# Optimization experiments

Measured on AMD Instinct MI355X. Metric: run time of the kernel, lower is better.

The kernel has to match this reference:

```python
import jax, jax.numpy as jnp
import numpy as np

EPS = 0.01          # layer_norm_epsilon from Gpt2Config
ROPE_THETA = 10000.0


def _rms_norm(x, w, eps=EPS):
    # RmsNorm over the last (head_size) axis, computed in fp32
    var = jnp.mean(jnp.square(x.astype(jnp.float32)), axis=-1, keepdims=True)
    return (x.astype(jnp.float32) * jax.lax.rsqrt(var + eps)).astype(x.dtype) * w


def _rope_cos_sin(seq_len, head_size, dtype):
    # default (NeoX/llama-style) rotary embeddings over the full head dim
    inv_freq = 1.0 / (ROPE_THETA ** (jnp.arange(0, head_size, 2, dtype=jnp.float32) / head_size))
    ang = jnp.arange(seq_len, dtype=jnp.float32)[:, None] * inv_freq[None, :]   # [S, D/2]
    cos = jnp.concatenate([jnp.cos(ang), jnp.cos(ang)], axis=-1).astype(dtype)  # [S, D]
    sin = jnp.concatenate([jnp.sin(ang), jnp.sin(ang)], axis=-1).astype(dtype)
    return cos, sin


def _rotate_half(x):
    half = x.shape[-1] // 2
    return jnp.concatenate([-x[..., half:], x[..., :half]], axis=-1)


def _apply_rope(x, cos, sin):
    # x: [B, S, H, D]; cos/sin: [S, D]
    return x * cos[None, :, None, :] + _rotate_half(x) * sin[None, :, None, :]


def setup_inputs() -> dict:
    key = jax.random.key(0)
    ks = jax.random.split(key, 3)
    B, S, E, H, D = 4, 2048, 2048, 16, 128
    x = jax.random.normal(ks[0], (B, S, E), dtype=jnp.float32)
    w_qkv = jax.random.normal(ks[1], (E, 3, H, D), dtype=jnp.float32) * 0.02
    w_proj = jax.random.normal(ks[2], (H, D, E), dtype=jnp.float32) * 0.02
    q_norm_w = jnp.ones((D,), dtype=jnp.float32)
    k_norm_w = jnp.ones((D,), dtype=jnp.float32)
    return {"x": x, "w_qkv": w_qkv, "w_proj": w_proj,
            "q_norm_w": q_norm_w, "k_norm_w": k_norm_w}


def reference(x, w_qkv, w_proj, q_norm_w, k_norm_w):
    B, S, E = x.shape
    _, _, H, D = w_qkv.shape

    # fused QKV projection (no bias)
    qkv = jnp.einsum('bse,ekhd->kbshd', x, w_qkv)  # [3, B, S, H, D]
    q, k, v = qkv[0], qkv[1], qkv[2]

    # qk RmsNorm over head_size
    q = _rms_norm(q, q_norm_w)
    k = _rms_norm(k, k_norm_w)

    # rotary embeddings
    cos, sin = _rope_cos_sin(S, D, x.dtype)
    q = _apply_rope(q, cos, sin)
    k = _apply_rope(k, cos, sin)

    # scaled dot-product attention, upcast to fp32, causal mask
    scale = 1.0 / jnp.sqrt(jnp.float32(D))
    scores = jnp.einsum('bshd,bthd->bhst', q.astype(jnp.float32),
                        k.astype(jnp.float32)) * scale        # [B, H, S, S]
    causal = jnp.arange(S)[:, None] >= jnp.arange(S)[None, :]  # [S, S]
    scores = jnp.where(causal[None, None], scores, jnp.float32(-1e9))
    attn = jax.nn.softmax(scores, axis=-1).astype(x.dtype)

    out = jnp.einsum('bhst,bthd->bshd', attn, v)               # [B, S, H, D]
    y = jnp.einsum('bshd,hde->bse', out, w_proj)               # output projection
    return y
```

## Files before the change

### kernel.cpp

```cpp
#include <hip/hip_runtime.h>
#include <hip/hip_bf16.h>
#include <math.h>

typedef unsigned short u16;
typedef __attribute__((ext_vector_type(8))) short short8;
typedef __attribute__((ext_vector_type(4))) float f32x4;
typedef __attribute__((ext_vector_type(4))) unsigned short ushort4v;
typedef __attribute__((ext_vector_type(8))) unsigned short ushort8v;

#define DEV static __device__ __forceinline__

DEV u16 f2bf(float f) {
    unsigned int x = __builtin_bit_cast(unsigned int, f);
    x += 0x7fffu + ((x >> 16) & 1u);
    return (u16)(x >> 16);
}
DEV float bf2f(u16 u) {
    unsigned int x = ((unsigned int)u) << 16;
    return __builtin_bit_cast(float, x);
}
DEV unsigned int pk_bf_trunc(float lo, float hi) {
    return __builtin_amdgcn_perm(__builtin_bit_cast(unsigned int, hi),
                                 __builtin_bit_cast(unsigned int, lo), 0x07060302u);
}

DEV void gl_lds16(const u16* g, u16* l) {
    __builtin_amdgcn_global_load_lds(
        (const __attribute__((address_space(1))) void*)g,
        (__attribute__((address_space(3))) void*)l, 16, 0, 0);
}

DEV short8 ldsv(const u16* p) { return *(const short8*)p; }

__global__ __launch_bounds__(256) void k_x2bf(
    const float* __restrict__ in, u16* __restrict__ out)
{
    int idx = blockIdx.x * 256 + threadIdx.x;
    const float4* p = (const float4*)in + (size_t)idx * 2;
    float4 a = p[0], b = p[1];
    ushort8v v;
    v[0] = f2bf(a.x); v[1] = f2bf(a.y); v[2] = f2bf(a.z); v[3] = f2bf(a.w);
    v[4] = f2bf(b.x); v[5] = f2bf(b.y); v[6] = f2bf(b.z); v[7] = f2bf(b.w);
    *(ushort8v*)(out + (size_t)idx * 8) = v;
}

__global__ __launch_bounds__(256) void k_transpose_bf16(
    const float* __restrict__ in, u16* __restrict__ out, int R, int C)
{
    __shared__ u16 t[64][72];
    int r0 = blockIdx.y * 64, c0 = blockIdx.x * 64;
    int tid = threadIdx.x;
    for (int i = 0; i < 4; ++i) {
        int u = tid + i * 256;
        int r = u >> 4, c4 = (u & 15) * 4;
        const float4 v = *(const float4*)(in + (size_t)(r0 + r) * C + c0 + c4);
        t[c4 + 0][r] = f2bf(v.x); t[c4 + 1][r] = f2bf(v.y);
        t[c4 + 2][r] = f2bf(v.z); t[c4 + 3][r] = f2bf(v.w);
    }
    __syncthreads();
    for (int i = 0; i < 4; ++i) {
        int u = tid + i * 256;
        int c = u >> 4, r4 = (u & 15) * 4;
        ushort4v v;
        v[0] = t[c][r4]; v[1] = t[c][r4 + 1]; v[2] = t[c][r4 + 2]; v[3] = t[c][r4 + 3];
        *(ushort4v*)(out + (size_t)(c0 + c) * R + r0 + r4) = v;
    }
}

template <int MODE>
__global__ __launch_bounds__(512, 2) void k_gemm256(
    const u16* __restrict__ A, const u16* __restrict__ Bt,
    u16* __restrict__ outQ, u16* __restrict__ outK, u16* __restrict__ outV,
    float* __restrict__ outF, int M, int N, int K)
{
    __shared__ u16 sA[2][2][128 * 64];
    __shared__ u16 sB[2][2][128 * 64];
    const int tid = threadIdx.x;
    const int lane = tid & 63, wid = tid >> 6;
    const int wm = wid >> 2, wn = wid & 3;
    const int lm = lane & 15, lq = lane >> 4;
    const int row0 = blockIdx.y * 256, col0 = blockIdx.x * 256;

    const int rl = lane >> 3;
    const int clog = (lane & 7) ^ rl;
    const u16* gA = A  + (size_t)(row0 + rl) * K + clog * 8;
    const u16* gB = Bt + (size_t)(col0 + rl) * K + clog * 8;
    const int rg = wid * 16;

    auto stA = [&](int bb, int h, int kt) {
        const u16* g = gA + (size_t)(h * 128 + rg) * K + (size_t)kt * 64;
        u16* l = &sA[bb][h][rg * 64];
        gl_lds16(g, l);
        gl_lds16(g + (size_t)8 * K, l + 512);
    };
    auto stB = [&](int bb, int h, int kt) {
        const u16* g = gB + (size_t)(h * 128 + rg) * K + (size_t)kt * 64;
        u16* l = &sB[bb][h][rg * 64];
        gl_lds16(g, l);
        gl_lds16(g + (size_t)8 * K, l + 512);
    };

    const int sw  = lm & 7;
    const int axr = lm * 64;
    const int bxr = ((wn & 1) * 64 + lm) * 64;
    const int co0 = ((lq ^ sw) << 3);
    const int co1 = (((lq | 4) ^ sw) << 3);

    f32x4 acc[8][4];
#pragma unroll
    for (int a = 0; a < 8; ++a)
#pragma unroll
        for (int b = 0; b < 4; ++b) acc[a][b] = (f32x4){0.f, 0.f, 0.f, 0.f};

    short8 af[4][2], bf[4][2];
    const int NT = K >> 6;

    stB(0, 0, 0); stB(0, 1, 0); stA(0, 0, 0); stA(0, 1, 0);
    stB(1, 0, 1); stB(1, 1, 1);
    asm volatile("s_waitcnt vmcnt(4)" ::: "memory");
    __builtin_amdgcn_s_barrier();

    auto tile_step = [&](int T, int buf) {
        const u16* pA = &sA[buf][wm][0];
        const u16* pB = &sB[buf][wn >> 1][0];
        const int nb = buf ^ 1;
        const bool p1ok = (T + 1 < NT);
        const bool p2ok = (T + 2 < NT);

#pragma unroll
        for (int t = 0; t < 4; ++t) {
            af[t][0] = ldsv(pA + axr + t * 1024 + co0);
            af[t][1] = ldsv(pA + axr + t * 1024 + co1);
        }
#pragma unroll
        for (int j = 0; j < 2; ++j) {
            bf[j][0] = ldsv(pB + bxr + j * 1024 + co0);
            bf[j][1] = ldsv(pB + bxr + j * 1024 + co1);
        }
        if (p1ok) stA(nb, 0, T + 1);
        asm volatile("s_waitcnt lgkmcnt(8)" ::: "memory");
        __builtin_amdgcn_s_barrier();
        asm volatile("s_waitcnt lgkmcnt(0)" ::: "memory");
        __builtin_amdgcn_s_setprio(1);
#pragma unroll
        for (int t = 0; t < 4; ++t)
#pragma unroll
            for (int j = 0; j < 2; ++j)
#pragma unroll
                for (int kk = 0; kk < 2; ++kk)
                    acc[t][j] = __builtin_amdgcn_mfma_f32_16x16x32_bf16(
                        af[t][kk], bf[j][kk], acc[t][j], 0, 0, 0);
        __builtin_amdgcn_s_setprio(0);
        __builtin_amdgcn_s_barrier();

#pragma unroll
        for (int j = 0; j < 2; ++j) {
            bf[2 + j][0] = ldsv(pB + bxr + (2 + j) * 1024 + co0);
            bf[2 + j][1] = ldsv(pB + bxr + (2 + j) * 1024 + co1);
        }
        if (p1ok) stA(nb, 1, T + 1);
        __builtin_amdgcn_s_barrier();
        asm volatile("s_waitcnt lgkmcnt(0)" ::: "memory");
        __builtin_amdgcn_s_setprio(1);
#pragma unroll
        for (int t = 0; t < 4; ++t)
#pragma unroll
            for (int j = 0; j < 2; ++j)
#pragma unroll
                for (int kk = 0; kk < 2; ++kk)
                    acc[t][2 + j] = __builtin_amdgcn_mfma_f32_16x16x32_bf16(
                        af[t][kk], bf[2 + j][kk], acc[t][2 + j], 0, 0, 0);
        __builtin_amdgcn_s_setprio(0);
        __builtin_amdgcn_s_barrier();

#pragma unroll
        for (int t = 0; t < 4; ++t) {
            af[t][0] = ldsv(pA + axr + (4 + t) * 1024 + co0);
            af[t][1] = ldsv(pA + axr + (4 + t) * 1024 + co1);
        }
        if (p2ok) stB(buf, 0, T + 2);
        __builtin_amdgcn_s_barrier();
        asm volatile("s_waitcnt lgkmcnt(0)" ::: "memory");
        __builtin_amdgcn_s_setprio(1);
#pragma unroll
        for (int t = 0; t < 4; ++t)
#pragma unroll
            for (int j = 0; j < 2; ++j)
#pragma unroll
                for (int kk = 0; kk < 2; ++kk)
                    acc[4 + t][2 + j] = __builtin_amdgcn_mfma_f32_16x16x32_bf16(
                        af[t][kk], bf[2 + j][kk], acc[4 + t][2 + j], 0, 0, 0);
        __builtin_amdgcn_s_setprio(0);
        __builtin_amdgcn_s_barrier();

        if (p2ok) {
            stB(buf, 1, T + 2);
            asm volatile("s_waitcnt vmcnt(4)" ::: "memory");
        } else {
            asm volatile("s_waitcnt vmcnt(0)" ::: "memory");
        }
        __builtin_amdgcn_s_barrier();
        __builtin_amdgcn_s_setprio(1);
#pragma unroll
        for (int t = 0; t < 4; ++t)
#pragma unroll
            for (int j = 0; j < 2; ++j)
#pragma unroll
                for (int kk = 0; kk < 2; ++kk)
                    acc[4 + t][j] = __builtin_amdgcn_mfma_f32_16x16x32_bf16(
                        af[t][kk], bf[j][kk], acc[4 + t][j], 0, 0, 0);
        __builtin_amdgcn_s_setprio(0);
        __builtin_amdgcn_s_barrier();
    };

    for (int T = 0; T < NT; T += 2) {
        tile_step(T, 0);
        tile_step(T + 1, 1);
    }
    asm volatile("s_waitcnt vmcnt(0)" ::: "memory");

    if (MODE == 0) {
        int k3 = col0 >> 11;
        u16* dst = (k3 == 0) ? outQ : (k3 == 1) ? outK : outV;
#pragma unroll
        for (int it = 0; it < 8; ++it)
#pragma unroll
            for (int jt = 0; jt < 4; ++jt) {
                int c = col0 + wn * 64 + jt * 16 + lm;
                int hd = c & 2047, h = hd >> 7, d = hd & 127;
#pragma unroll
                for (int i = 0; i < 4; ++i) {
                    int r = row0 + wm * 128 + it * 16 + lq * 4 + i;
                    int b = r >> 11, s = r & 2047;
                    dst[((size_t)(b * 16 + h) * 2048 + s) * 128 + d] = f2bf(acc[it][jt][i]);
                }
            }
    } else {
#pragma unroll
        for (int it = 0; it < 8; ++it)
#pragma unroll
            for (int jt = 0; jt < 4; ++jt) {
                int c = col0 + wn * 64 + jt * 16 + lm;
#pragma unroll
                for (int i = 0; i < 4; ++i) {
                    int r = row0 + wm * 128 + it * 16 + lq * 4 + i;
                    outF[(size_t)r * N + c] = acc[it][jt][i];
                }
            }
    }
}

__global__ __launch_bounds__(256) void k_normrope(
    u16* __restrict__ X, const float* __restrict__ w, float oscale)
{
    int row = blockIdx.x * 4 + (threadIdx.x >> 6);
    int t = threadIdx.x & 63;
    int s = row & 2047;
    u16* p = X + (size_t)row * 128;
    float x0 = bf2f(p[t]), x1 = bf2f(p[t + 64]);
    float ss = x0 * x0 + x1 * x1;
    for (int m = 1; m < 64; m <<= 1) ss += __shfl_xor(ss, m);
    float r = rsqrtf(ss * (1.0f / 128.0f) + 0.01f);
    float a = x0 * r * w[t];
    float b = x1 * r * w[t + 64];
    float freq = exp2f(-13.287712379549449f * ((float)t * (1.0f / 64.0f)));
    float ang = (float)s * freq;
    float sn, c;
    sincosf(ang, &sn, &c);
    p[t]      = f2bf((a * c - b * sn) * oscale);
    p[t + 64] = f2bf((b * c + a * sn) * oscale);
}

__global__ __launch_bounds__(256) void k_vtrans(
    const u16* __restrict__ Vh, u16* __restrict__ Vt, int S)
{
    __shared__ u16 t[128][68];
    int bh = blockIdx.y, s0 = blockIdx.x * 64;
    int tid = threadIdx.x;
    const u16* src = Vh + ((size_t)bh * S + s0) * 128;
    for (int i = 0; i < 4; ++i) {
        int u = tid + i * 256;
        int r = u >> 4, c8 = (u & 15) * 8;
        ushort8v v = *(const ushort8v*)(src + (size_t)r * 128 + c8);
        for (int j = 0; j < 8; ++j) t[c8 + j][r] = v[j];
    }
    __syncthreads();
    u16* dst = Vt + (size_t)bh * 128 * S + s0;
    for (int i = 0; i < 8; ++i) {
        int u = tid + i * 256;
        int d = u >> 4, s4 = (u & 15) * 4;
        ushort4v v;
        v[0] = t[d][s4]; v[1] = t[d][s4 + 1]; v[2] = t[d][s4 + 2]; v[3] = t[d][s4 + 3];
        *(ushort4v*)(dst + (size_t)d * S + s4) = v;
    }
}

template <bool DIAG>
DEV void flash_core(int kb, int lq, int lm, int qcol,
                    const u16* __restrict__ sKf, const u16* __restrict__ sVf,
                    const short8 qf[4], f32x4 oacc[8],
                    float& mprev, float& lsum, u16* __restrict__ sPw,
                    f32x4 sacc[4])
{
    for (int nt = 0; nt < 4; ++nt) sacc[nt] = (f32x4){0.f, 0.f, 0.f, 0.f};
    for (int nt = 0; nt < 4; ++nt)
        for (int kc = 0; kc < 4; ++kc) {
            short8 kf = *(const short8*)(sKf + (nt * 16 + lm) * 128 +
                                         (((kc * 4 + lq) ^ lm) << 3));
            sacc[nt] = __builtin_amdgcn_mfma_f32_16x16x32_bf16(kf, qf[kc], sacc[nt], 0, 0, 0);
        }
}

DEV void flash_softmax_pv(int lq, int lm,
                          const u16* __restrict__ sVf,
                          f32x4 oacc[8], float& mprev, float& lsum,
                          u16* __restrict__ sPw, f32x4 sacc[4])
{
    float mx = sacc[0][0];
    for (int nt = 0; nt < 4; ++nt)
        for (int i = 0; i < 4; ++i) mx = fmaxf(mx, sacc[nt][i]);
    mx = fmaxf(mx, __shfl_xor(mx, 16));
    mx = fmaxf(mx, __shfl_xor(mx, 32));
    float mnew = fmaxf(mprev, mx);
    float alpha = exp2f(mprev - mnew);
    float rs = 0.0f;
    for (int nt = 0; nt < 4; ++nt)
        for (int i = 0; i < 4; ++i) {
            float pv = exp2f(sacc[nt][i] - mnew);
            sacc[nt][i] = pv;
            rs += pv;
        }
    rs += __shfl_xor(rs, 16);
    rs += __shfl_xor(rs, 32);
    lsum = lsum * alpha + rs;
    mprev = mnew;

    for (int nt = 0; nt < 4; ++nt) {
        uint2 pk;
        pk.x = pk_bf_trunc(sacc[nt][0], sacc[nt][1]);
        pk.y = pk_bf_trunc(sacc[nt][2], sacc[nt][3]);
        *(uint2*)(sPw + lm * 64 +
                  ((((nt << 1) + (lq >> 1)) ^ (lm & 7)) << 3) + ((lq & 1) << 2)) = pk;
    }

    float alphar[4];
    for (int i = 0; i < 4; ++i) alphar[i] = __shfl(alpha, lq * 4 + i, 16);
    for (int f = 0; f < 8; ++f)
        for (int i = 0; i < 4; ++i) oacc[f][i] *= alphar[i];

    short8 pf[2];
    for (int kc = 0; kc < 2; ++kc)
        pf[kc] = *(const short8*)(sPw + lm * 64 + (((kc * 4 + lq) ^ (lm & 7)) << 3));
    for (int f = 0; f < 8; ++f)
        for (int kc = 0; kc < 2; ++kc) {
            short8 vf = *(const short8*)(sVf + (f * 16 + lm) * 64 +
                                         (((kc * 4 + lq) ^ (lm & 7)) << 3));
            oacc[f] = __builtin_amdgcn_mfma_f32_16x16x32_bf16(pf[kc], vf, oacc[f], 0, 0, 0);
        }
}

__global__ __launch_bounds__(256, 4) void k_flash(
    const u16* __restrict__ Qh, const u16* __restrict__ Kh,
    const u16* __restrict__ Vt, u16* __restrict__ ctx, int S)
{
    __shared__ u16 sK[64 * 128];
    __shared__ u16 sV[128 * 64];
    __shared__ u16 sP[4 * 16 * 64];
    int bh = blockIdx.y;
    int b = bh >> 4, h = bh & 15;
    int tid = threadIdx.x, lane = tid & 63, w = tid >> 6;
    int lm = lane & 15, lq = lane >> 4;
    const u16* qbase = Qh + (size_t)bh * S * 128;
    u16* sPw = &sP[w * 16 * 64];

    int kck = lm ^ (w * 4 + lq);
    const u16* kg = Kh + (size_t)bh * S * 128 + (size_t)(w * 4 + lq) * 128 + kck * 8;
    int hi3 = lane >> 3, c3 = lane & 7;
    int vck = c3 ^ (hi3 & 7);
    const u16* vg = Vt + (size_t)bh * 128 * S + (size_t)(w * 8 + hi3) * S + vck * 8;

    auto stageK = [&](int kb) {
        const u16* g = kg + (size_t)kb * (64 * 128);
        for (int i = 0; i < 4; ++i)
            gl_lds16(g + i * (16 * 128), sK + (i * 16 + w * 4) * 128);
    };
    auto stageV = [&](int kb) {
        const u16* g = vg + kb * 64;
        for (int i = 0; i < 4; ++i)
            gl_lds16(g + (size_t)(i * 32) * S, sV + (i * 32 + w * 8) * 64);
    };

    for (int half = 0; half < 2; ++half) {
        int qi = half == 0 ? 31 - (int)blockIdx.x : (int)blockIdx.x;

        if (half == 1) __syncthreads();

        int q0 = qi * 64 + w * 16;
        short8 qf[4];
        for (int kc = 0; kc < 4; ++kc)
            qf[kc] = *(const short8*)(qbase + (size_t)(q0 + lm) * 128 + kc * 32 + lq * 8);

        f32x4 oacc[8];
        for (int f = 0; f < 8; ++f) oacc[f] = (f32x4){0.f, 0.f, 0.f, 0.f};
        float mprev = -1e30f, lsum = 0.0f;
        int qcol = q0 + lm;

        stageK(0);
        stageV(0);
        __syncthreads();

        f32x4 sacc[4];
        for (int kb = 0; kb < qi; ++kb) {
            flash_core<false>(kb, lq, lm, qcol, sK, sV, qf, oacc, mprev, lsum, sPw, sacc);
            __syncthreads();
            stageK(kb + 1);
            flash_softmax_pv(lq, lm, sV, oacc, mprev, lsum, sPw, sacc);
            __syncthreads();
            stageV(kb + 1);
        }
        flash_core<true>(qi, lq, lm, qcol, sK, sV, qf, oacc, mprev, lsum, sPw, sacc);
        for (int nt = 0; nt < 4; ++nt)
            for (int i = 0; i < 4; ++i) {
                int kv = qi * 64 + nt * 16 + lq * 4 + i;
                if (kv > qcol) sacc[nt][i] = -1e30f;
            }
        __syncthreads();
        flash_softmax_pv(lq, lm, sV, oacc, mprev, lsum, sPw, sacc);

        float linv[4];
        for (int i = 0; i < 4; ++i)
            linv[i] = 1.0f / __shfl(lsum, lq * 4 + i, 16);
        u16* obase = ctx + (size_t)b * S * 2048 + h * 128;
        for (int f = 0; f < 8; ++f) {
            int d = f * 16 + lm;
            for (int i = 0; i < 4; ++i) {
                int s = qi * 64 + w * 16 + lq * 4 + i;
                obase[(size_t)s * 2048 + d] = f2bf(oacc[f][i] * linv[i]);
            }
        }
    }
}

extern "C" void kernel_launch(void* const* d_in, const int* in_sizes, int n_in,
                              void* d_out, int out_size, void* d_ws, size_t ws_size,
                              hipStream_t stream)
{
    const float* x        = (const float*)d_in[0];
    const float* w_qkv    = (const float*)d_in[1];
    const float* w_proj   = (const float*)d_in[2];
    const float* q_norm_w = (const float*)d_in[3];
    const float* k_norm_w = (const float*)d_in[4];
    float* out = (float*)d_out;

    const int B = 4, S = 2048, E = 2048, H = 16;
    const int M  = B * S;
    const int N1 = 3 * E;
    const int N2 = E;
    const float QSCALE = 0.12751743f;

    char* ws = (char*)d_ws;
    size_t off = 0;
    auto alloc = [&](size_t bytes) {
        char* p = ws + off;
        off += (bytes + 255) & ~(size_t)255;
        return p;
    };
    u16* Wpt  = (u16*)alloc((size_t)E * E * 2);
    char* regR = alloc((size_t)M * N1 * 2);
    u16* Wqt  = (u16*)regR;
    u16* ctxp = (u16*)regR;
    u16* Qh = (u16*)alloc((size_t)M * E * 2);
    u16* Kh = (u16*)alloc((size_t)M * E * 2);
    u16* Vh = (u16*)alloc((size_t)M * E * 2);
    char* regV = alloc((size_t)M * E * 2);
    u16* xb = (u16*)regV;
    u16* Vt = (u16*)regV;

    k_x2bf<<<(M * E) / (256 * 8), 256, 0, stream>>>(x, xb);
    k_transpose_bf16<<<dim3(N1 / 64, E / 64), 256, 0, stream>>>(w_qkv, Wqt, E, N1);
    k_transpose_bf16<<<dim3(N2 / 64, E / 64), 256, 0, stream>>>(w_proj, Wpt, E, N2);
    k_gemm256<0><<<dim3(N1 / 256, M / 256), 512, 0, stream>>>(
        xb, Wqt, Qh, Kh, Vh, nullptr, M, N1, E);
    k_normrope<<<(B * H * S) / 4, 256, 0, stream>>>(Qh, q_norm_w, QSCALE);
    k_normrope<<<(B * H * S) / 4, 256, 0, stream>>>(Kh, k_norm_w, 1.0f);
    k_vtrans<<<dim3(S / 64, B * H), 256, 0, stream>>>(Vh, Vt, S);
    k_flash<<<dim3(16, B * H), 256, 0, stream>>>(Qh, Kh, Vt, ctxp, S);
    k_gemm256<1><<<dim3(N2 / 256, M / 256), 512, 0, stream>>>(
        ctxp, Wpt, nullptr, nullptr, nullptr, out, M, N2, E);
}
```

Baseline: 600.9 us.

## Double-buffer K/V tiles in flash attention with vmcnt-based prefetch pipeline

The flash-attention kernel now keeps two LDS buffers each for the K and V tiles and prefetches tile t+2 while tile t is being computed. Explicit vmcnt waits and raw barriers replace the __syncthreads pairs. MFMA sections are wrapped in s_setprio to raise wave priority during matrix work, and launch bounds drop from 4 to 2 blocks per CU to fit the doubled LDS. The goal is to hide global-to-LDS latency behind compute, at the cost of lower occupancy and hand-counted vmcnt values that must match the number of outstanding loads.

```diff
diff --git a/kernel.cpp b/kernel.cpp
--- a/kernel.cpp
+++ b/kernel.cpp
@@ -303,12 +303,14 @@
                     f32x4 sacc[4])
 {
     for (int nt = 0; nt < 4; ++nt) sacc[nt] = (f32x4){0.f, 0.f, 0.f, 0.f};
+    __builtin_amdgcn_s_setprio(1);
     for (int nt = 0; nt < 4; ++nt)
         for (int kc = 0; kc < 4; ++kc) {
             short8 kf = *(const short8*)(sKf + (nt * 16 + lm) * 128 +
                                          (((kc * 4 + lq) ^ lm) << 3));
             sacc[nt] = __builtin_amdgcn_mfma_f32_16x16x32_bf16(kf, qf[kc], sacc[nt], 0, 0, 0);
         }
+    __builtin_amdgcn_s_setprio(0);
 }
 
 DEV void flash_softmax_pv(int lq, int lm,
@@ -351,20 +353,22 @@
     short8 pf[2];
     for (int kc = 0; kc < 2; ++kc)
         pf[kc] = *(const short8*)(sPw + lm * 64 + (((kc * 4 + lq) ^ (lm & 7)) << 3));
+    __builtin_amdgcn_s_setprio(1);
     for (int f = 0; f < 8; ++f)
         for (int kc = 0; kc < 2; ++kc) {
             short8 vf = *(const short8*)(sVf + (f * 16 + lm) * 64 +
                                          (((kc * 4 + lq) ^ (lm & 7)) << 3));
             oacc[f] = __builtin_amdgcn_mfma_f32_16x16x32_bf16(pf[kc], vf, oacc[f], 0, 0, 0);
         }
-}
-
-__global__ __launch_bounds__(256, 4) void k_flash(
+    __builtin_amdgcn_s_setprio(0);
+}
+
+__global__ __launch_bounds__(256, 2) void k_flash(
     const u16* __restrict__ Qh, const u16* __restrict__ Kh,
     const u16* __restrict__ Vt, u16* __restrict__ ctx, int S)
 {
-    __shared__ u16 sK[64 * 128];
-    __shared__ u16 sV[128 * 64];
+    __shared__ u16 sK[2][64 * 128];
+    __shared__ u16 sV[2][128 * 64];
     __shared__ u16 sP[4 * 16 * 64];
     int bh = blockIdx.y;
     int b = bh >> 4, h = bh & 15;
@@ -381,13 +385,15 @@
 
     auto stageK = [&](int kb) {
         const u16* g = kg + (size_t)kb * (64 * 128);
+        u16* d = sK[kb & 1];
         for (int i = 0; i < 4; ++i)
-            gl_lds16(g + i * (16 * 128), sK + (i * 16 + w * 4) * 128);
+            gl_lds16(g + i * (16 * 128), d + (i * 16 + w * 4) * 128);
     };
     auto stageV = [&](int kb) {
         const u16* g = vg + kb * 64;
+        u16* d = sV[kb & 1];
         for (int i = 0; i < 4; ++i)
-            gl_lds16(g + (size_t)(i * 32) * S, sV + (i * 32 + w * 8) * 64);
+            gl_lds16(g + (size_t)(i * 32) * S, d + (i * 32 + w * 8) * 64);
     };
 
     for (int half = 0; half < 2; ++half) {
@@ -404,28 +410,42 @@
         for (int f = 0; f < 8; ++f) oacc[f] = (f32x4){0.f, 0.f, 0.f, 0.f};
         float mprev = -1e30f, lsum = 0.0f;
         int qcol = q0 + lm;
-
-        stageK(0);
-        stageV(0);
-        __syncthreads();
+        const int last = qi;
+
+        stageK(0); stageV(0);
+        if (last >= 1) { stageK(1); stageV(1); }
 
         f32x4 sacc[4];
-        for (int kb = 0; kb < qi; ++kb) {
-            flash_core<false>(kb, lq, lm, qcol, sK, sV, qf, oacc, mprev, lsum, sPw, sacc);
-            __syncthreads();
-            stageK(kb + 1);
-            flash_softmax_pv(lq, lm, sV, oacc, mprev, lsum, sPw, sacc);
-            __syncthreads();
-            stageV(kb + 1);
-        }
-        flash_core<true>(qi, lq, lm, qcol, sK, sV, qf, oacc, mprev, lsum, sPw, sacc);
-        for (int nt = 0; nt < 4; ++nt)
-            for (int i = 0; i < 4; ++i) {
-                int kv = qi * 64 + nt * 16 + lq * 4 + i;
-                if (kv > qcol) sacc[nt][i] = -1e30f;
+        for (int t = 0; t <= last; ++t) {
+            const int tb = t & 1;
+            const bool h1 = (t + 1 <= last), h2 = (t + 2 <= last);
+
+            if (h1) asm volatile("s_waitcnt vmcnt(12)" ::: "memory");
+            else    asm volatile("s_waitcnt vmcnt(4)"  ::: "memory");
+            __builtin_amdgcn_s_barrier();
+
+            flash_core<false>(t, lq, lm, qcol, sK[tb], sV[tb], qf,
+                              oacc, mprev, lsum, sPw, sacc);
+            if (t == last) {
+                for (int nt = 0; nt < 4; ++nt)
+                    for (int i = 0; i < 4; ++i) {
+                        int kv = t * 64 + nt * 16 + lq * 4 + i;
+                        if (kv > qcol) sacc[nt][i] = -1e30f;
+                    }
             }
-        __syncthreads();
-        flash_softmax_pv(lq, lm, sV, oacc, mprev, lsum, sPw, sacc);
+            __builtin_amdgcn_s_barrier();
+            if (h2) stageK(t + 2);
+
+            if (h1) {
+                if (h2) asm volatile("s_waitcnt vmcnt(12)" ::: "memory");
+                else    asm volatile("s_waitcnt vmcnt(8)"  ::: "memory");
+            } else      asm volatile("s_waitcnt vmcnt(0)"  ::: "memory");
+            __builtin_amdgcn_s_barrier();
+
+            flash_softmax_pv(lq, lm, sV[tb], oacc, mprev, lsum, sPw, sacc);
+            __builtin_amdgcn_s_barrier();
+            if (h2) stageV(t + 2);
+        }
 
         float linv[4];
         for (int i = 0; i < 4; ++i)
```

Measured after the change: 615.3 us. +2.4%, slower.
